# Performance work log

Hardware: AMD Instinct MI355X
Metric: run time of the kernel (lower is better)

## Reference

```python
import jax, jax.numpy as jnp
import numpy as np

B, M, D, N, P = 8, 2048, 1024, 128, 16


def setup_inputs() -> dict:
    key = jax.random.key(0)
    k1, k2, k3 = jax.random.split(key, 3)
    x = jax.random.normal(k1, (B, M, D), dtype=jnp.float32)
    # kaiming-uniform-ish scale for phi
    phi = jax.random.normal(k2, (D, N, P), dtype=jnp.float32) * (1.0 / np.sqrt(D))
    # per-expert dense layer d -> d
    w_exp = jax.random.normal(k3, (N, D, D), dtype=jnp.float32) * (1.0 / np.sqrt(D))
    b_exp = jnp.zeros((N, D), dtype=jnp.float32)
    return {"x": x, "phi": phi, "w_exp": w_exp, "b_exp": b_exp}


def reference(x, phi, w_exp, b_exp):
    b, m, d = x.shape
    n, p = phi.shape[1], phi.shape[2]
    # routing logits: (b, m, n, p)
    logits = jnp.einsum('bmd,dnp->bmnp', x, phi)
    # dispatch: softmax over the batch dim (dim=0), faithful to the source
    dispatch = jax.nn.softmax(logits, axis=0)
    # combine: softmax over all slots (n*p) jointly
    combine = jax.nn.softmax(logits.reshape(b, m, n * p), axis=-1).reshape(b, m, n, p)
    # dispatch tokens to slots: (b, n, p, d)
    slots = jnp.einsum('bmd,bmnp->bnpd', x, dispatch)
    # per-expert dense layer (MultiExpertLayer): d -> d with bias
    expert_out = jnp.einsum('bnpd,nde->bnpe', slots, w_exp) + b_exp[None, :, None, :]
    # combine slot outputs back to tokens: (b, m, d)
    out = jnp.einsum('bnpd,bmnp->bmd', expert_out, combine)
    return out
```

## Files before the change

### kernel.cpp

```cpp
#include <hip/hip_runtime.h>

#define B_ 8
#define M_ 2048
#define D_ 1024
#define N_ 128
#define P_ 16
#define NP_ 2048
#define BM_ 16384

typedef __attribute__((ext_vector_type(8))) short bf16x8;
typedef __attribute__((ext_vector_type(4))) float f32x4;
typedef unsigned short ushort_t;

__device__ __forceinline__ ushort_t f2bf(float f) {
    union { float f; unsigned u; } v; v.f = f;
    unsigned r = v.u + 0x7fffu + ((v.u >> 16) & 1u);
    return (ushort_t)(r >> 16);
}

__device__ __forceinline__ void async_copy16(const void* g, void* l) {
    __builtin_amdgcn_global_load_lds((const __attribute__((address_space(1))) void*)g,
                                     (__attribute__((address_space(3))) void*)l, 16, 0, 0);
}

template<int OUT_BF16, int HAS_BIAS>
__global__ __launch_bounds__(256, 2)
void gemm_tn(const ushort_t* __restrict__ A, const ushort_t* __restrict__ Bm,
             void* __restrict__ C, const float* __restrict__ bias,
             int K, int lda, int ldb,
             long a_bs, long b_bs, long c_bs, long bias_bs,
             long ci_hi, long ci_lo, long cj_hi, long cj_lo)
{
    __shared__ __align__(16) ushort_t As[128 * 64];
    __shared__ __align__(16) ushort_t Bs[128 * 64];

    const int t = threadIdx.x;
    const int lane = t & 63;
    const int w = t >> 6;
    const int wr = w >> 1, wc = w & 1;
    const int quad = lane >> 4, lr = lane & 15;
    const int i0 = blockIdx.y * 128;
    const int j0 = blockIdx.x * 128;
    const int batch = blockIdx.z;

    const ushort_t* Ab = A + (size_t)batch * a_bs;
    const ushort_t* Bb = Bm + (size_t)batch * b_bs;

    f32x4 acc[4][4];
#pragma unroll
    for (int a = 0; a < 4; ++a)
#pragma unroll
        for (int b = 0; b < 4; ++b)
            acc[a][b] = (f32x4){0.f, 0.f, 0.f, 0.f};

    for (int kt = 0; kt < K; kt += 64) {
#pragma unroll
        for (int c = 0; c < 4; ++c) {
            int idx = c * 256 + t;
            int row = idx >> 3, slot = idx & 7;
            int chunk = slot ^ (row & 7);
            const ushort_t* ga = Ab + (size_t)(i0 + row) * lda + kt + chunk * 8;
            const ushort_t* gb = Bb + (size_t)(j0 + row) * ldb + kt + chunk * 8;
            char* la = (char*)As + c * 4096 + w * 1024;
            char* lb = (char*)Bs + c * 4096 + w * 1024;
            async_copy16(ga, la);
            async_copy16(gb, lb);
        }
        __syncthreads();

#pragma unroll
        for (int ks = 0; ks < 2; ++ks) {
            bf16x8 af[4], bfr[4];
#pragma unroll
            for (int mt = 0; mt < 4; ++mt) {
                int row = wr * 64 + mt * 16 + lr;
                int chunk = ks * 4 + quad;
                int slot = chunk ^ (row & 7);
                af[mt] = *(const bf16x8*)((const char*)As + row * 128 + slot * 16);
            }
#pragma unroll
            for (int nt = 0; nt < 4; ++nt) {
                int col = wc * 64 + nt * 16 + lr;
                int chunk = ks * 4 + quad;
                int slot = chunk ^ (col & 7);
                bfr[nt] = *(const bf16x8*)((const char*)Bs + col * 128 + slot * 16);
            }
#pragma unroll
            for (int mt = 0; mt < 4; ++mt)
#pragma unroll
                for (int nt = 0; nt < 4; ++nt)
                    acc[mt][nt] = __builtin_amdgcn_mfma_f32_16x16x32_bf16(af[mt], bfr[nt], acc[mt][nt], 0, 0, 0);
        }
        __syncthreads();
    }

    long cbase = (long)batch * c_bs;
#pragma unroll
    for (int mt = 0; mt < 4; ++mt) {
#pragma unroll
        for (int nt = 0; nt < 4; ++nt) {
            int j = j0 + wc * 64 + nt * 16 + lr;
            long jpart = (long)(j >> 4) * cj_hi + (long)(j & 15) * cj_lo;
            f32x4 v = acc[mt][nt];
#pragma unroll
            for (int r = 0; r < 4; ++r) {
                int i = i0 + wr * 64 + mt * 16 + quad * 4 + r;
                float val = v[r];
                if (HAS_BIAS) val += bias[(size_t)batch * bias_bs + i];
                long addr = cbase + (long)(i >> 4) * ci_hi + (long)(i & 15) * ci_lo + jpart;
                if (OUT_BF16) ((ushort_t*)C)[addr] = f2bf(val);
                else          ((float*)C)[addr] = val;
            }
        }
    }
}

__global__ __launch_bounds__(256)
void cast_bf16(const float* __restrict__ in, ushort_t* __restrict__ out)
{
    size_t i = (size_t)blockIdx.x * 256 + threadIdx.x;
    float4 f = *(const float4*)(in + i * 4);
    union { ushort_t us[4]; uint2 v; } pk;
    pk.us[0] = f2bf(f.x); pk.us[1] = f2bf(f.y);
    pk.us[2] = f2bf(f.z); pk.us[3] = f2bf(f.w);
    *(uint2*)(out + i * 4) = pk.v;
}

__global__ __launch_bounds__(256)
void transpose_cast(const float* __restrict__ in, ushort_t* __restrict__ out,
                    int ldi, int ldo, long in_bs, long out_bs)
{
    __shared__ float tile[64][65];
    int t = threadIdx.x;
    const float* ib = in + (size_t)blockIdx.z * in_bs;
    ushort_t* ob = out + (size_t)blockIdx.z * out_bs;
    int c0 = blockIdx.x * 64, r0 = blockIdx.y * 64;
#pragma unroll
    for (int it = 0; it < 16; ++it) {
        int r = it * 4 + (t >> 6);
        int c = t & 63;
        tile[r][c] = ib[(size_t)(r0 + r) * ldi + c0 + c];
    }
    __syncthreads();
#pragma unroll
    for (int it = 0; it < 8; ++it) {
        int rr = it * 8 + (t >> 5);
        int cc = (t & 31) * 2;
        ushort2 pk;
        pk.x = f2bf(tile[cc][rr]);
        pk.y = f2bf(tile[cc + 1][rr]);
        *(ushort2*)(ob + (size_t)(c0 + rr) * ldo + r0 + cc) = pk;
    }
}

__global__ __launch_bounds__(256)
void softmax_b(const float* __restrict__ L, ushort_t* __restrict__ dT)
{
    int t = threadIdx.x;
    int n0 = blockIdx.x * 64, m0 = blockIdx.y * 32;
    int ncol = t & 63, mb = t >> 6;

    float vals[8][8];
#pragma unroll
    for (int b = 0; b < 8; ++b)
#pragma unroll
        for (int it = 0; it < 8; ++it) {
            int m = m0 + it * 4 + mb;
            vals[b][it] = L[(size_t)b * (M_ * (size_t)NP_) + (size_t)m * NP_ + n0 + ncol];
        }

    float inv[8];
#pragma unroll
    for (int it = 0; it < 8; ++it) {
        float mx = vals[0][it];
#pragma unroll
        for (int b = 1; b < 8; ++b) mx = fmaxf(mx, vals[b][it]);
        float s = 0.f;
#pragma unroll
        for (int b = 0; b < 8; ++b) { vals[b][it] = __expf(vals[b][it] - mx); s += vals[b][it]; }
        inv[it] = 1.f / s;
    }

    __shared__ float tile[64][33];
#pragma unroll
    for (int b = 0; b < 8; ++b) {
        __syncthreads();
#pragma unroll
        for (int it = 0; it < 8; ++it)
            tile[ncol][it * 4 + mb] = vals[b][it] * inv[it];
        __syncthreads();
#pragma unroll
        for (int it2 = 0; it2 < 4; ++it2) {
            int rr = it2 * 16 + (t >> 4);
            int cc = (t & 15) * 2;
            ushort2 pk;
            pk.x = f2bf(tile[rr][cc]);
            pk.y = f2bf(tile[rr][cc + 1]);
            *(ushort2*)(dT + (size_t)b * (NP_ * (size_t)M_) + (size_t)(n0 + rr) * M_ + m0 + cc) = pk;
        }
    }
}

__global__ __launch_bounds__(256)
void softmax_np(const float* __restrict__ L, ushort_t* __restrict__ Cb)
{
    int row = blockIdx.x;
    const float* Lr = L + (size_t)row * NP_;
    int t = threadIdx.x;
    int w = t >> 6, lane = t & 63;

    float v[8];
    float4 u0 = *(const float4*)(Lr + t * 8);
    float4 u1 = *(const float4*)(Lr + t * 8 + 4);
    v[0] = u0.x; v[1] = u0.y; v[2] = u0.z; v[3] = u0.w;
    v[4] = u1.x; v[5] = u1.y; v[6] = u1.z; v[7] = u1.w;

    float mx = v[0];
#pragma unroll
    for (int j = 1; j < 8; ++j) mx = fmaxf(mx, v[j]);
#pragma unroll
    for (int off = 32; off > 0; off >>= 1) mx = fmaxf(mx, __shfl_xor(mx, off));

    __shared__ float red[8];
    if (lane == 0) red[w] = mx;
    __syncthreads();
    mx = fmaxf(fmaxf(red[0], red[1]), fmaxf(red[2], red[3]));

    float s = 0.f;
#pragma unroll
    for (int j = 0; j < 8; ++j) { v[j] = __expf(v[j] - mx); s += v[j]; }
#pragma unroll
    for (int off = 32; off > 0; off >>= 1) s += __shfl_xor(s, off);
    if (lane == 0) red[4 + w] = s;
    __syncthreads();
    s = red[4] + red[5] + red[6] + red[7];
    float is = 1.f / s;

    union { ushort_t us[8]; int4 v4; } pk;
#pragma unroll
    for (int j = 0; j < 8; ++j) pk.us[j] = f2bf(v[j] * is);
    *(int4*)(Cb + (size_t)row * NP_ + t * 8) = pk.v4;
}

extern "C" void kernel_launch(void* const* d_in, const int* in_sizes, int n_in,
                              void* d_out, int out_size, void* d_ws, size_t ws_size,
                              hipStream_t stream)
{
    (void)in_sizes; (void)n_in; (void)out_size; (void)ws_size;
    const float* x     = (const float*)d_in[0];
    const float* phi   = (const float*)d_in[1];
    const float* w_exp = (const float*)d_in[2];
    const float* b_exp = (const float*)d_in[3];
    float* out = (float*)d_out;
    char* ws = (char*)d_ws;

    ushort_t* xbf   = (ushort_t*)(ws + 0);
    ushort_t* xT    = (ushort_t*)(ws + 33554432);
    ushort_t* phiT  = (ushort_t*)(ws + 67108864);
    float*    L     = (float*)   (ws + 71303168);
    ushort_t* dT    = (ushort_t*)(ws + 205520896);
    ushort_t* wT    = (ushort_t*)(ws + 0);
    ushort_t* cmb   = (ushort_t*)(ws + 272629760);
    ushort_t* slots = (ushort_t*)(ws + 339738624);
    ushort_t* eoT   = (ushort_t*)(ws + 373293056);

    cast_bf16<<<dim3(BM_ * D_ / 1024), 256, 0, stream>>>(x, xbf);
    transpose_cast<<<dim3(NP_ / 64, D_ / 64, 1), 256, 0, stream>>>(phi, phiT, NP_, D_, 0, 0);
    transpose_cast<<<dim3(D_ / 64, M_ / 64, B_), 256, 0, stream>>>(x, xT, D_, M_,
        (long)M_ * D_, (long)D_ * M_);
    gemm_tn<0, 0><<<dim3(NP_ / 128, BM_ / 128, 1), 256, 0, stream>>>(
        xbf, phiT, L, nullptr, D_, D_, D_,
        0, 0, 0, 0,
        16L * NP_, NP_, 16, 1);
    softmax_b<<<dim3(NP_ / 64, M_ / 32), 256, 0, stream>>>(L, dT);
    softmax_np<<<dim3(B_ * M_), 256, 0, stream>>>(L, cmb);
    gemm_tn<1, 0><<<dim3(D_ / 128, NP_ / 128, B_), 256, 0, stream>>>(
        dT, xT, slots, nullptr, M_, M_, M_,
        (long)NP_ * M_, (long)D_ * M_, (long)P_ * D_, 0,
        (long)B_ * P_ * D_, D_, 16, 1);
    transpose_cast<<<dim3(D_ / 64, D_ / 64, N_), 256, 0, stream>>>(w_exp, wT, D_, D_,
        (long)D_ * D_, (long)D_ * D_);
    gemm_tn<1, 1><<<dim3(1, D_ / 128, N_), 256, 0, stream>>>(
        wT, slots, eoT, b_exp, D_, D_, D_,
        (long)D_ * D_, (long)B_ * P_ * D_, 16, D_,
        16L * NP_, NP_, (long)D_ * NP_, 1);
    gemm_tn<0, 0><<<dim3(D_ / 128, M_ / 128, B_), 256, 0, stream>>>(
        cmb, eoT, out, nullptr, NP_, NP_, NP_,
        (long)M_ * NP_, (long)D_ * NP_, (long)M_ * D_, 0,
        16L * D_, D_, 16, 1);
}
```

Before: 1.198 ms.

## Fuse expert weight transpose-cast into GEMM, bf16 logits, merge x prep kernels

Replaces the separate transpose_cast of the 512MB fp32 expert weights plus its GEMM with one kernel that loads fp32 W tiles into LDS, converts and transposes them in shared memory, then runs MFMA. Logits are stored as bf16 instead of fp32, halving their write and read traffic in the two softmax kernels. The x cast and x transpose are merged into one kernel that reads x once. The costs are lower precision in the routing logits before the softmaxes, and extra LDS use plus barriers per k-step in the expert GEMM.

```diff
diff --git a/kernel.cpp b/kernel.cpp
--- a/kernel.cpp
+++ b/kernel.cpp
@@ -16,6 +16,11 @@
     union { float f; unsigned u; } v; v.f = f;
     unsigned r = v.u + 0x7fffu + ((v.u >> 16) & 1u);
     return (ushort_t)(r >> 16);
+}
+
+__device__ __forceinline__ float bf2f(ushort_t u) {
+    union { unsigned u; float f; } v; v.u = ((unsigned)u) << 16;
+    return v.f;
 }
 
 __device__ __forceinline__ void async_copy16(const void* g, void* l) {
@@ -115,15 +120,146 @@
     }
 }
 
+__global__ __launch_bounds__(256, 2)
+void gemm_expert(const float* __restrict__ W, const ushort_t* __restrict__ S,
+                 ushort_t* __restrict__ EO, const float* __restrict__ bias)
+{
+    __shared__ __align__(16) ushort_t As[128 * 64];
+    __shared__ __align__(16) ushort_t Bs[128 * 64];
+    __shared__ __align__(16) float    Wf[64 * 128];
+
+    const int t = threadIdx.x;
+    const int lane = t & 63;
+    const int w = t >> 6;
+    const int wr = w >> 1, wc = w & 1;
+    const int quad = lane >> 4, lr = lane & 15;
+    const int i0 = blockIdx.x * 128;
+    const int n  = blockIdx.y;
+
+    const float* Wn = W + (size_t)n * D_ * D_;
+    const ushort_t* Sn = S + (size_t)n * 128 * D_;
+
+    f32x4 acc[4][4];
+#pragma unroll
+    for (int a = 0; a < 4; ++a)
+#pragma unroll
+        for (int b = 0; b < 4; ++b)
+            acc[a][b] = (f32x4){0.f, 0.f, 0.f, 0.f};
+
+    const int e_tr = t & 127, half_tr = t >> 7;
+
+    for (int kt = 0; kt < D_; kt += 64) {
+#pragma unroll
+        for (int c = 0; c < 4; ++c) {
+            int idx = c * 256 + t;
+            int row = idx >> 3, slot = idx & 7;
+            int chunk = slot ^ (row & 7);
+            const ushort_t* gb = Sn + (size_t)row * D_ + kt + chunk * 8;
+            char* lb = (char*)Bs + c * 4096 + w * 1024;
+            async_copy16(gb, lb);
+        }
+#pragma unroll
+        for (int c = 0; c < 8; ++c) {
+            int idx = c * 256 + t;
+            int krow = idx >> 5, c16 = idx & 31;
+            const float* gw = Wn + (size_t)(kt + krow) * D_ + i0 + c16 * 4;
+            char* lw = (char*)Wf + c * 4096 + w * 1024;
+            async_copy16(gw, lw);
+        }
+        __syncthreads();
+
+#pragma unroll
+        for (int cc = 0; cc < 4; ++cc) {
+            int chunk = half_tr * 4 + cc;
+            float f[8];
+#pragma unroll
+            for (int j = 0; j < 8; ++j)
+                f[j] = Wf[(chunk * 8 + j) * 128 + e_tr];
+            union { ushort_t us[8]; bf16x8 v; } pk;
+#pragma unroll
+            for (int j = 0; j < 8; ++j) pk.us[j] = f2bf(f[j]);
+            int slot = chunk ^ (e_tr & 7);
+            *(bf16x8*)((char*)As + e_tr * 128 + slot * 16) = pk.v;
+        }
+        __syncthreads();
+
+#pragma unroll
+        for (int ks = 0; ks < 2; ++ks) {
+            bf16x8 af[4], bfr[4];
+#pragma unroll
+            for (int mt = 0; mt < 4; ++mt) {
+                int row = wr * 64 + mt * 16 + lr;
+                int chunk = ks * 4 + quad;
+                int slot = chunk ^ (row & 7);
+                af[mt] = *(const bf16x8*)((const char*)As + row * 128 + slot * 16);
+            }
+#pragma unroll
+            for (int nt = 0; nt < 4; ++nt) {
+                int col = wc * 64 + nt * 16 + lr;
+                int chunk = ks * 4 + quad;
+                int slot = chunk ^ (col & 7);
+                bfr[nt] = *(const bf16x8*)((const char*)Bs + col * 128 + slot * 16);
+            }
+#pragma unroll
+            for (int mt = 0; mt < 4; ++mt)
+#pragma unroll
+                for (int nt = 0; nt < 4; ++nt)
+                    acc[mt][nt] = __builtin_amdgcn_mfma_f32_16x16x32_bf16(af[mt], bfr[nt], acc[mt][nt], 0, 0, 0);
+        }
+        __syncthreads();
+    }
+
+#pragma unroll
+    for (int mt = 0; mt < 4; ++mt) {
+#pragma unroll
+        for (int nt = 0; nt < 4; ++nt) {
+            int j = wc * 64 + nt * 16 + lr;
+            int bidx = j >> 4, p = j & 15;
+            f32x4 v = acc[mt][nt];
+#pragma unroll
+            for (int r = 0; r < 4; ++r) {
+                int i = i0 + wr * 64 + mt * 16 + quad * 4 + r;
+                float val = v[r] + bias[(size_t)n * D_ + i];
+                EO[(size_t)bidx * ((size_t)D_ * NP_) + (size_t)i * NP_ + n * 16 + p] = f2bf(val);
+            }
+        }
+    }
+}
+
 __global__ __launch_bounds__(256)
-void cast_bf16(const float* __restrict__ in, ushort_t* __restrict__ out)
-{
-    size_t i = (size_t)blockIdx.x * 256 + threadIdx.x;
-    float4 f = *(const float4*)(in + i * 4);
-    union { ushort_t us[4]; uint2 v; } pk;
-    pk.us[0] = f2bf(f.x); pk.us[1] = f2bf(f.y);
-    pk.us[2] = f2bf(f.z); pk.us[3] = f2bf(f.w);
-    *(uint2*)(out + i * 4) = pk.v;
+void prep_x(const float* __restrict__ x, ushort_t* __restrict__ xbf,
+            ushort_t* __restrict__ xT)
+{
+    __shared__ float tile[64][65];
+    int t = threadIdx.x;
+    int b = blockIdx.z;
+    int d0 = blockIdx.x * 64, m0 = blockIdx.y * 64;
+    const float* ib = x + (size_t)b * M_ * D_;
+
+#pragma unroll
+    for (int it = 0; it < 4; ++it) {
+        int row = it * 16 + (t >> 4);
+        int c4 = (t & 15) * 4;
+        float4 f = *(const float4*)(ib + (size_t)(m0 + row) * D_ + d0 + c4);
+        union { ushort_t us[4]; uint2 v; } pk;
+        pk.us[0] = f2bf(f.x); pk.us[1] = f2bf(f.y);
+        pk.us[2] = f2bf(f.z); pk.us[3] = f2bf(f.w);
+        *(uint2*)(xbf + ((size_t)b * M_ + m0 + row) * D_ + d0 + c4) = pk.v;
+        tile[row][c4]     = f.x;
+        tile[row][c4 + 1] = f.y;
+        tile[row][c4 + 2] = f.z;
+        tile[row][c4 + 3] = f.w;
+    }
+    __syncthreads();
+#pragma unroll
+    for (int it = 0; it < 8; ++it) {
+        int rr = it * 8 + (t >> 5);
+        int cc = (t & 31) * 2;
+        ushort2 pk;
+        pk.x = f2bf(tile[cc][rr]);
+        pk.y = f2bf(tile[cc + 1][rr]);
+        *(ushort2*)(xT + (size_t)b * D_ * M_ + (size_t)(d0 + rr) * M_ + m0 + cc) = pk;
+    }
 }
 
 __global__ __launch_bounds__(256)
@@ -154,7 +290,7 @@
 }
 
 __global__ __launch_bounds__(256)
-void softmax_b(const float* __restrict__ L, ushort_t* __restrict__ dT)
+void softmax_b(const ushort_t* __restrict__ L, ushort_t* __restrict__ dT)
 {
     int t = threadIdx.x;
     int n0 = blockIdx.x * 64, m0 = blockIdx.y * 32;
@@ -166,7 +302,7 @@
 #pragma unroll
         for (int it = 0; it < 8; ++it) {
             int m = m0 + it * 4 + mb;
-            vals[b][it] = L[(size_t)b * (M_ * (size_t)NP_) + (size_t)m * NP_ + n0 + ncol];
+            vals[b][it] = bf2f(L[(size_t)b * (M_ * (size_t)NP_) + (size_t)m * NP_ + n0 + ncol]);
         }
 
     float inv[8];
@@ -202,18 +338,18 @@
 }
 
 __global__ __launch_bounds__(256)
-void softmax_np(const float* __restrict__ L, ushort_t* __restrict__ Cb)
+void softmax_np(const ushort_t* __restrict__ L, ushort_t* __restrict__ Cb)
 {
     int row = blockIdx.x;
-    const float* Lr = L + (size_t)row * NP_;
+    const ushort_t* Lr = L + (size_t)row * NP_;
     int t = threadIdx.x;
     int w = t >> 6, lane = t & 63;
 
+    union { int4 v4; ushort_t us[8]; } ld;
+    ld.v4 = *(const int4*)(Lr + t * 8);
     float v[8];
-    float4 u0 = *(const float4*)(Lr + t * 8);
-    float4 u1 = *(const float4*)(Lr + t * 8 + 4);
-    v[0] = u0.x; v[1] = u0.y; v[2] = u0.z; v[3] = u0.w;
-    v[4] = u1.x; v[5] = u1.y; v[6] = u1.z; v[7] = u1.w;
+#pragma unroll
+    for (int j = 0; j < 8; ++j) v[j] = bf2f(ld.us[j]);
 
     float mx = v[0];
 #pragma unroll
@@ -257,18 +393,15 @@
     ushort_t* xbf   = (ushort_t*)(ws + 0);
     ushort_t* xT    = (ushort_t*)(ws + 33554432);
     ushort_t* phiT  = (ushort_t*)(ws + 67108864);
-    float*    L     = (float*)   (ws + 71303168);
-    ushort_t* dT    = (ushort_t*)(ws + 205520896);
-    ushort_t* wT    = (ushort_t*)(ws + 0);
-    ushort_t* cmb   = (ushort_t*)(ws + 272629760);
-    ushort_t* slots = (ushort_t*)(ws + 339738624);
-    ushort_t* eoT   = (ushort_t*)(ws + 373293056);
-
-    cast_bf16<<<dim3(BM_ * D_ / 1024), 256, 0, stream>>>(x, xbf);
+    ushort_t* L     = (ushort_t*)(ws + 71303168);
+    ushort_t* dT    = (ushort_t*)(ws + 138412032);
+    ushort_t* cmb   = (ushort_t*)(ws + 205520896);
+    ushort_t* slots = (ushort_t*)(ws + 272629760);
+    ushort_t* eoT   = (ushort_t*)(ws + 306184192);
+
+    prep_x<<<dim3(D_ / 64, M_ / 64, B_), 256, 0, stream>>>(x, xbf, xT);
     transpose_cast<<<dim3(NP_ / 64, D_ / 64, 1), 256, 0, stream>>>(phi, phiT, NP_, D_, 0, 0);
-    transpose_cast<<<dim3(D_ / 64, M_ / 64, B_), 256, 0, stream>>>(x, xT, D_, M_,
-        (long)M_ * D_, (long)D_ * M_);
-    gemm_tn<0, 0><<<dim3(NP_ / 128, BM_ / 128, 1), 256, 0, stream>>>(
+    gemm_tn<1, 0><<<dim3(NP_ / 128, BM_ / 128, 1), 256, 0, stream>>>(
         xbf, phiT, L, nullptr, D_, D_, D_,
         0, 0, 0, 0,
         16L * NP_, NP_, 16, 1);
@@ -278,12 +411,7 @@
         dT, xT, slots, nullptr, M_, M_, M_,
         (long)NP_ * M_, (long)D_ * M_, (long)P_ * D_, 0,
         (long)B_ * P_ * D_, D_, 16, 1);
-    transpose_cast<<<dim3(D_ / 64, D_ / 64, N_), 256, 0, stream>>>(w_exp, wT, D_, D_,
-        (long)D_ * D_, (long)D_ * D_);
-    gemm_tn<1, 1><<<dim3(1, D_ / 128, N_), 256, 0, stream>>>(
-        wT, slots, eoT, b_exp, D_, D_, D_,
-        (long)D_ * D_, (long)B_ * P_ * D_, 16, D_,
-        16L * NP_, NP_, (long)D_ * NP_, 1);
+    gemm_expert<<<dim3(D_ / 128, N_), 256, 0, stream>>>(w_exp, slots, eoT, b_exp);
     gemm_tn<0, 0><<<dim3(D_ / 128, M_ / 128, B_), 256, 0, stream>>>(
         cmb, eoT, out, nullptr, NP_, NP_, NP_,
         (long)M_ * NP_, (long)D_ * NP_, (long)M_ * D_, 0,
```

Result: faster. 1.066 ms (-11.0%).
